# Kernel tuning notes

Hardware: AMD Instinct MI355X
Metric: run time of the kernel (lower is better)

## Reference

```python
import jax, jax.numpy as jnp
import numpy as np

B, H_IMG, W_IMG = 8, 64, 64
C, HEADS, SR, MSG = 128, 4, 4, 4
N0 = H_IMG * W_IMG


def _linear(x, w, b):
    return x @ w.T + b


def _layernorm(x, g, b, eps=1e-5):
    mu = jnp.mean(x, -1, keepdims=True)
    var = jnp.mean(jnp.square(x - mu), -1, keepdims=True)
    return (x - mu) * jax.lax.rsqrt(var + eps) * g + b


def _conv2d(x, w, b, stride, pad, groups=1):
    y = jax.lax.conv_general_dilated(
        x, w, (stride, stride), [(pad, pad), (pad, pad)],
        dimension_numbers=("NCHW", "OIHW", "NCHW"), feature_group_count=groups)
    return y + b[None, :, None, None]


def setup_inputs():
    key = jax.random.key(0)
    ks = jax.random.split(key, 16)
    def nrm(k, shape, std=0.02):
        return jax.random.normal(k, shape, jnp.float32) * std
    z = lambda *s: jnp.zeros(s, jnp.float32)
    return {
        "x": jax.random.normal(ks[0], (B, N0, C), jnp.float32),
        "msg_tokens": jax.random.normal(ks[1], (B, MSG, C), jnp.float32),
        "Wq": nrm(ks[2], (C, C)), "bq": z(C),
        "sr1_w": nrm(ks[3], (C, C, 4, 4), float(np.sqrt(2.0 / (16 * C)))), "sr1_b": z(C),
        "ln1_g": jnp.ones((C,), jnp.float32), "ln1_b": z(C),
        "sr2_w": nrm(ks[4], (C, C, 2, 2), float(np.sqrt(2.0 / (4 * C)))), "sr2_b": z(C),
        "ln2_g": jnp.ones((C,), jnp.float32), "ln2_b": z(C),
        "kv1_w": nrm(ks[5], (C, C)), "kv1_b": z(C),
        "kv2_w": nrm(ks[6], (C, C)), "kv2_b": z(C),
        "lc1_w": nrm(ks[7], (C // 2, 1, 3, 3), float(np.sqrt(2.0 / 9.0))), "lc1_b": z(C // 2),
        "lc2_w": nrm(ks[8], (C // 2, 1, 3, 3), float(np.sqrt(2.0 / 9.0))), "lc2_b": z(C // 2),
        "proj_w": nrm(ks[9], (C, C)), "proj_b": z(C),
        "H": H_IMG, "W": W_IMG,
    }


def reference(x, msg_tokens, Wq, bq, sr1_w, sr1_b, ln1_g, ln1_b,
              sr2_w, sr2_b, ln2_g, ln2_b, kv1_w, kv1_b, kv2_w, kv2_b,
              lc1_w, lc1_b, lc2_w, lc2_b, proj_w, proj_b, H, W):
    Bsz, _, Cc = x.shape
    m = msg_tokens.shape[1]
    h = HEADS
    dh = Cc // h
    scale = dh ** -0.5
    x_q = jnp.concatenate([x, msg_tokens], axis=1)       # [B, N, C]
    N = x_q.shape[1]
    q = _linear(x_q, Wq, bq).reshape(Bsz, N, h, dh).transpose(0, 2, 1, 3)  # [B,h,N,dh]
    x_img = x.transpose(0, 2, 1).reshape(Bsz, Cc, H, W)

    def branch(sr_w, sr_b, ln_g, ln_b, kv_w, kv_b, lc_w, lc_b, q_half, stride):
        Hr, Wr = H // stride, W // stride
        L = Hr * Wr
        # spatial reduction conv -> tokens
        xr = _conv2d(x_img, sr_w, sr_b, stride, 0).reshape(Bsz, Cc, L).transpose(0, 2, 1)
        # message tokens pass through the SR conv via summed weights
        msg_r = jnp.einsum('bnc,oc->bno', msg_tokens, sr_w.sum((-1, -2))) + sr_b
        xk = jax.nn.gelu(_layernorm(jnp.concatenate([xr, msg_r], 1), ln_g, ln_b), approximate=False)
        kv = _linear(xk, kv_w, kv_b).reshape(Bsz, L + m, 2, h // 2, dh).transpose(2, 0, 3, 1, 4)
        k, v = kv[0], kv[1]                               # [B, h/2, L+m, dh]
        attn = jax.nn.softmax(jnp.einsum('bhnd,bhld->bhnl', q_half, k) * scale, axis=-1)
        # fused depthwise conv on the spatial part of V (message tokens bypass)
        v_flat = v.transpose(0, 2, 1, 3).reshape(Bsz, L + m, Cc // 2).transpose(0, 2, 1)  # [B,C/2,L+m]
        lc = _conv2d(v_flat[:, :, :L].reshape(Bsz, Cc // 2, Hr, Wr), lc_w, lc_b, 1, 1,
                     groups=Cc // 2).reshape(Bsz, Cc // 2, L)
        v_add = jnp.concatenate([lc, v_flat[:, :, L:]], axis=2)
        v = v + v_add.reshape(Bsz, h // 2, dh, L + m).transpose(0, 1, 3, 2)
        return jnp.einsum('bhnl,bhld->bhnd', attn, v).transpose(0, 2, 1, 3).reshape(Bsz, N, Cc // 2)

    x1 = branch(sr1_w, sr1_b, ln1_g, ln1_b, kv1_w, kv1_b, lc1_w, lc1_b, q[:, :h // 2], SR)
    x2 = branch(sr2_w, sr2_b, ln2_g, ln2_b, kv2_w, kv2_b, lc2_w, lc2_b, q[:, h // 2:], SR // 2)
    out = _linear(jnp.concatenate([x1, x2], -1), proj_w, proj_b)
    out = x_q + out                                       # identity = x_q, drop_path = Identity
    return out[:, :-m], out[:, -m:]
```

## Files before the change

### kernel.cpp

```cpp
#include <hip/hip_runtime.h>
#include <math.h>

#define BB 8
#define CC 128
#define N0 4096
#define MSGN 4
#define NTOT 4100
#define IMG 64
#define NPAD 4112
#define QTILES 257
#define LMP1 320
#define LMP2 1088

#define OFF_WFQ    0
#define OFF_WFKV1  8192
#define OFF_WFKV2  16384
#define OFF_WFPROJ 24576
#define OFF_WFSR1  32768
#define OFF_WFSR2  163840
#define OFF_QH     196608
#define OFF_XK1    2301952
#define OFF_XK2    2435072
#define OFF_KV1O   2961408
#define OFF_KV2O   3227648
#define OFF_KH1    4280320
#define OFF_VT1    4362240
#define OFF_KH2    4444160
#define OFF_VT2    4722688
#define OFF_XP0    5001216
#define OFF_XP1    7102464
#define OFF_L0     2301952
#define OFF_L1     2433280

typedef _Float16 half8v __attribute__((ext_vector_type(8)));
typedef _Float16 half4v __attribute__((ext_vector_type(4)));
typedef float f32x4 __attribute__((ext_vector_type(4)));

__device__ __forceinline__ size_t af_idx(int m, int k, int Kc) {
    return ((size_t)((m >> 4) * Kc + (k >> 5)) * 64 + ((k >> 3) & 3) * 16 + (m & 15)) * 8 + (k & 7);
}

__global__ void prep_weights(const float* __restrict__ Wq, const float* __restrict__ kv1,
                             const float* __restrict__ kv2, const float* __restrict__ proj,
                             const float* __restrict__ sr1w, const float* __restrict__ sr2w,
                             float* __restrict__ ws, _Float16* __restrict__ Qh) {
    int u = blockIdx.x * blockDim.x + threadIdx.x;
    if (u >= 49152) {
        int idx = u - 49152;
        if (idx >= BB * 4 * (NPAD - NTOT) * 32) return;
        int d = idx & 31;
        int rest = idx >> 5;
        int n = NTOT + rest % (NPAD - NTOT);
        int rest2 = rest / (NPAD - NTOT);
        int hg = rest2 & 3;
        int b = rest2 >> 2;
        Qh[((size_t)(b * 4 + hg) * NPAD + n) * 32 + d] = (_Float16)0.f;
        return;
    }
    int seg, base;
    const float* w = nullptr;
    _Float16* dst;
    if (u < 2048)        { seg = 0; base = u;          w = Wq;   dst = (_Float16*)(ws + OFF_WFQ); }
    else if (u < 4096)   { seg = 0; base = u - 2048;   w = kv1;  dst = (_Float16*)(ws + OFF_WFKV1); }
    else if (u < 6144)   { seg = 0; base = u - 4096;   w = kv2;  dst = (_Float16*)(ws + OFF_WFKV2); }
    else if (u < 8192)   { seg = 0; base = u - 6144;   w = proj; dst = (_Float16*)(ws + OFF_WFPROJ); }
    else if (u < 40960)  { seg = 1; base = u - 8192;   w = sr1w; dst = (_Float16*)(ws + OFF_WFSR1); }
    else                 { seg = 2; base = u - 40960;  w = sr2w; dst = (_Float16*)(ws + OFF_WFSR2); }
    int lane = base & 63;
    int t = (base >> 6) & 7;
    int kc = base >> 9;
    int n = t * 16 + (lane & 15);
    int k0 = kc * 32 + (lane >> 4) * 8;
    half8v val;
    #pragma unroll
    for (int j = 0; j < 8; ++j) {
        int k = k0 + j;
        float v;
        if (seg == 0) v = w[n * 128 + k];
        else if (seg == 1) v = w[(n * 128 + (k & 127)) * 16 + (k >> 7)];
        else v = w[(n * 128 + (k & 127)) * 4 + (k >> 7)];
        val[j] = (_Float16)v;
    }
    *(half8v*)(dst + (size_t)base * 8) = val;
}

template<int S, int WR, int LL, int LM, int KW>
__device__ __forceinline__ void sr_partial(
    int mtile, int kcbase, int lane, const float* __restrict__ x,
    const float* __restrict__ msg, const _Float16* __restrict__ Wf, f32x4 acc[8]) {
    int m15 = lane & 15, quadk = lane >> 4;
    int m = mtile * 16 + m15;
    bool valid = m < BB * LM;
    const float* base = x;
    bool isimg = false;
    if (valid) {
        int b = m / LM, tok = m - b * LM;
        if (tok < LL) {
            int hr = tok / WR, wr = tok - hr * WR;
            base = x + ((size_t)b * N0 + hr * S * IMG + wr * S) * 128;
            isimg = true;
        } else {
            base = msg + ((size_t)b * MSGN + (tok - LL)) * 128;
        }
    }
    const half8v* Bp = (const half8v*)Wf + lane;
    for (int kk = 0; kk < KW; ++kk) {
        int kc = kcbase + kk;
        int k0 = (kc * 4 + quadk) * 8;
        int c = k0 & 127, ij = k0 >> 7;
        half8v a;
        if (valid) {
            int off;
            if (isimg) {
                int ki = ij / S, kj = ij - ki * S;
                off = (ki * IMG + kj) * 128 + c;
            } else off = c;
            const float4* p4 = (const float4*)(base + off);
            float4 f0 = p4[0], f1 = p4[1];
            a[0] = (_Float16)f0.x; a[1] = (_Float16)f0.y; a[2] = (_Float16)f0.z; a[3] = (_Float16)f0.w;
            a[4] = (_Float16)f1.x; a[5] = (_Float16)f1.y; a[6] = (_Float16)f1.z; a[7] = (_Float16)f1.w;
        } else {
            #pragma unroll
            for (int j = 0; j < 8; ++j) a[j] = (_Float16)0.f;
        }
        #pragma unroll
        for (int t = 0; t < 8; ++t)
            acc[t] = __builtin_amdgcn_mfma_f32_16x16x32_f16(a, Bp[(size_t)(kc * 8 + t) * 64], acc[t], 0, 0, 0);
    }
}

__global__ __launch_bounds__(256) void input_gemms(
    const float* __restrict__ x, const float* __restrict__ msg,
    const _Float16* __restrict__ Wf1, const _Float16* __restrict__ Wf2,
    const float* __restrict__ b1, const float* __restrict__ g1, const float* __restrict__ be1,
    const float* __restrict__ b2, const float* __restrict__ g2, const float* __restrict__ be2,
    _Float16* __restrict__ XK1, _Float16* __restrict__ XK2,
    const _Float16* __restrict__ WfQ, const float* __restrict__ bq,
    _Float16* __restrict__ Qh) {
    __shared__ float red[4][2048];
    int tid = threadIdx.x;
    int lane = tid & 63, wave = tid >> 6;
    int bid = blockIdx.x;

    if (bid >= 646) {
        int mt = (bid - 646) * 4 + wave;
        int m15 = lane & 15, quadk = lane >> 4;
        int m = mt * 16 + m15;
        bool valid = m < BB * NTOT;
        const float* rowp = x;
        if (valid) {
            int b = m / NTOT, n = m - b * NTOT;
            rowp = (n < N0) ? (x + ((size_t)b * N0 + n) * 128)
                            : (msg + ((size_t)b * MSGN + (n - N0)) * 128);
        }
        const half8v* Bp = (const half8v*)WfQ + lane;
        f32x4 acc[8];
        #pragma unroll
        for (int t = 0; t < 8; ++t) acc[t] = (f32x4){0.f, 0.f, 0.f, 0.f};
        #pragma unroll
        for (int kc = 0; kc < 4; ++kc) {
            half8v a;
            if (valid) {
                const float4* p4 = (const float4*)(rowp + (kc * 4 + quadk) * 8);
                float4 f0 = p4[0], f1 = p4[1];
                a[0] = (_Float16)f0.x; a[1] = (_Float16)f0.y; a[2] = (_Float16)f0.z; a[3] = (_Float16)f0.w;
                a[4] = (_Float16)f1.x; a[5] = (_Float16)f1.y; a[6] = (_Float16)f1.z; a[7] = (_Float16)f1.w;
            } else {
                #pragma unroll
                for (int j = 0; j < 8; ++j) a[j] = (_Float16)0.f;
            }
            #pragma unroll
            for (int t = 0; t < 8; ++t)
                acc[t] = __builtin_amdgcn_mfma_f32_16x16x32_f16(a, Bp[(size_t)(kc * 8 + t) * 64], acc[t], 0, 0, 0);
        }
        int quad = lane >> 4, n15 = lane & 15;
        const float qscale = 0.17677669529663687f;
        #pragma unroll
        for (int r = 0; r < 4; ++r) {
            int mm = mt * 16 + quad * 4 + r;
            if (mm >= BB * NTOT) continue;
            int b = mm / NTOT, tok = mm - b * NTOT;
            #pragma unroll
            for (int t = 0; t < 8; ++t) {
                int n = t * 16 + n15;
                Qh[((size_t)(b * 4 + (n >> 5)) * NPAD + tok) * 32 + (n & 31)] =
                    (_Float16)((acc[t][r] + bq[n]) * qscale);
            }
        }
        return;
    }

    f32x4 acc[8];
    #pragma unroll
    for (int t = 0; t < 8; ++t) acc[t] = (f32x4){0.f, 0.f, 0.f, 0.f};
    const float* bias;
    const float* lng;
    const float* lnb;
    _Float16* outp;
    int mtile, Mv;
    if (bid < 132) {
        mtile = bid; Mv = 2080;
        sr_partial<4, 16, 256, 260, 16>(mtile, wave * 16, lane, x, msg, Wf1, acc);
        bias = b1; lng = g1; lnb = be1; outp = XK1;
    } else {
        mtile = bid - 132; Mv = 8224;
        sr_partial<2, 32, 1024, 1028, 4>(mtile, wave * 4, lane, x, msg, Wf2, acc);
        bias = b2; lng = g2; lnb = be2; outp = XK2;
    }
    int quad = lane >> 4, n15 = lane & 15;
    #pragma unroll
    for (int t = 0; t < 8; ++t)
        #pragma unroll
        for (int r = 0; r < 4; ++r)
            red[wave][(quad * 4 + r) * 128 + t * 16 + n15] = acc[t][r];
    __syncthreads();
    for (int e = tid; e < 2048; e += 256)
        red[0][e] = red[0][e] + red[1][e] + red[2][e] + red[3][e];
    __syncthreads();
    int r16 = tid >> 4, l16 = tid & 15;
    int m = mtile * 16 + r16;
    float v[8];
    float s = 0.f;
    #pragma unroll
    for (int j = 0; j < 8; ++j) { v[j] = red[0][r16 * 128 + j * 16 + l16] + bias[j * 16 + l16]; s += v[j]; }
    #pragma unroll
    for (int off = 1; off < 16; off <<= 1) s += __shfl_xor(s, off);
    float mu = s * (1.f / 128.f);
    float q = 0.f;
    #pragma unroll
    for (int j = 0; j < 8; ++j) { v[j] -= mu; q += v[j] * v[j]; }
    #pragma unroll
    for (int off = 1; off < 16; off <<= 1) q += __shfl_xor(q, off);
    float rs = rsqrtf(q * (1.f / 128.f) + 1e-5f);
    if (m < Mv) {
        #pragma unroll
        for (int j = 0; j < 8; ++j) {
            int n = j * 16 + l16;
            float y = v[j] * rs * lng[n] + lnb[n];
            y = 0.5f * y * (1.f + erff(y * 0.70710678118654752f));
            outp[af_idx(m, n, 4)] = (_Float16)y;
        }
    }
}

__global__ __launch_bounds__(256) void kv_gemm(
    const _Float16* __restrict__ XK1, const _Float16* __restrict__ XK2,
    const _Float16* __restrict__ Wf1, const _Float16* __restrict__ Wf2,
    const float* __restrict__ b1, const float* __restrict__ b2,
    float* __restrict__ o1, float* __restrict__ o2) {
    int lane = threadIdx.x & 63, wave = threadIdx.x >> 6;
    int t = blockIdx.x * 4 + wave;
    int lt;
    const half8v* Ap;
    const half8v* Bp;
    const float* bias;
    float* outp;
    if (t < 130) { lt = t;       Ap = (const half8v*)XK1 + (size_t)lt * 4 * 64 + lane; Bp = (const half8v*)Wf1 + lane; bias = b1; outp = o1; }
    else         { lt = t - 130; Ap = (const half8v*)XK2 + (size_t)lt * 4 * 64 + lane; Bp = (const half8v*)Wf2 + lane; bias = b2; outp = o2; }
    f32x4 acc[8];
    #pragma unroll
    for (int tt = 0; tt < 8; ++tt) acc[tt] = (f32x4){0.f, 0.f, 0.f, 0.f};
    #pragma unroll
    for (int kc = 0; kc < 4; ++kc) {
        half8v a = Ap[(size_t)kc * 64];
        #pragma unroll
        for (int tt = 0; tt < 8; ++tt)
            acc[tt] = __builtin_amdgcn_mfma_f32_16x16x32_f16(a, Bp[(size_t)(kc * 8 + tt) * 64], acc[tt], 0, 0, 0);
    }
    int quad = lane >> 4, n15 = lane & 15;
    #pragma unroll
    for (int r = 0; r < 4; ++r) {
        int m = lt * 16 + quad * 4 + r;
        #pragma unroll
        for (int tt = 0; tt < 8; ++tt)
            outp[(size_t)m * 128 + tt * 16 + n15] = acc[tt][r] + bias[tt * 16 + n15];
    }
}

__global__ void pack_kv(const float* __restrict__ kv1o, const float* __restrict__ kv2o,
                        const float* __restrict__ lc1w, const float* __restrict__ lc1b,
                        const float* __restrict__ lc2w, const float* __restrict__ lc2b,
                        _Float16* __restrict__ Kh1, _Float16* __restrict__ Vt1,
                        _Float16* __restrict__ Kh2, _Float16* __restrict__ Vt2) {
    int idx = blockIdx.x * 256 + threadIdx.x;
    const int T1 = BB * LMP1 * 64;
    const float* kv;
    const float* lcw;
    const float* lcb;
    _Float16* Kh;
    _Float16* Vt;
    int Wr, L, Lm, Lmp, li;
    if (idx < T1) { li = idx;      kv = kv1o; lcw = lc1w; lcb = lc1b; Kh = Kh1; Vt = Vt1; Wr = 16; L = 256;  Lm = 260;  Lmp = LMP1; }
    else          { li = idx - T1; kv = kv2o; lcw = lc2w; lcb = lc2b; Kh = Kh2; Vt = Vt2; Wr = 32; L = 1024; Lm = 1028; Lmp = LMP2; }
    int ch = li & 63;
    int rest = li >> 6;
    int n = rest % Lmp;
    int b = rest / Lmp;
    int h2 = ch >> 5, d = ch & 31;
    int Hr = L / Wr;
    float kval = 0.f, vnew = 0.f;
    if (n < Lm) {
        const float* kvb = kv + (size_t)b * Lm * 128;
        kval = kvb[(size_t)n * 128 + ch];
        float v = kvb[(size_t)n * 128 + 64 + ch];
        float add;
        if (n < L) {
            int hr = n / Wr, wr = n - hr * Wr;
            float sum = lcb[ch];
            #pragma unroll
            for (int ki = 0; ki < 3; ++ki)
                #pragma unroll
                for (int kj = 0; kj < 3; ++kj) {
                    int y = hr + ki - 1, xx = wr + kj - 1;
                    if ((unsigned)y < (unsigned)Hr && (unsigned)xx < (unsigned)Wr)
                        sum += lcw[ch * 9 + ki * 3 + kj] * kvb[((size_t)y * Wr + xx) * 128 + 64 + ch];
                }
            add = sum;
        } else {
            add = v;
        }
        vnew = v + add;
    }
    Kh[((size_t)(b * 2 + h2) * Lmp + n) * 32 + d] = (_Float16)kval;
    Vt[(size_t)(b * 2 + h2) * Lmp * 32 + (size_t)(n >> 2) * 128 + d * 4 + (n & 3)] = (_Float16)vnew;
}

__global__ __launch_bounds__(256) void attn_mfma(
    const _Float16* __restrict__ Qh,
    const _Float16* __restrict__ Kh1, const _Float16* __restrict__ Vt1,
    const _Float16* __restrict__ Kh2, const _Float16* __restrict__ Vt2,
    _Float16* __restrict__ XP0, _Float16* __restrict__ XP1,
    float* __restrict__ L0, float* __restrict__ L1) {
    int tid = threadIdx.x;
    int lane = tid & 63, wave = tid >> 6;
    int b = blockIdx.y;
    int z = blockIdx.z;
    int h2 = z & 1, h = z >> 1;
    int tile = blockIdx.x * 4 + wave;
    if (tile >= QTILES) return;
    int n0 = tile * 16;
    int q16 = lane & 15, quad = lane >> 4;
    const f32x4 zf = {0.f, 0.f, 0.f, 0.f};
    _Float16* xp = h ? XP1 : XP0;
    float* Lp = h ? L1 : L0;

    for (int br = 0; br < 2; ++br) {
        int Lmp = br ? LMP2 : LMP1;
        int k_lo = h ? (br ? 576 : 192) : 0;
        int k_hi = br ? (h ? 1088 : 576) : (h ? 320 : 192);
        const _Float16* kb = (br ? Kh2 : Kh1) + (size_t)(b * 2 + h2) * Lmp * 32;
        const _Float16* vb = (br ? Vt2 : Vt1) + (size_t)(b * 2 + h2) * Lmp * 32;
        int hg = br * 2 + h2;
        half8v qf = *(const half8v*)(Qh + ((size_t)(b * 4 + hg) * NPAD + n0 + q16) * 32 + quad * 8);
        f32x4 O0 = {0.f, 0.f, 0.f, 0.f}, O1 = {0.f, 0.f, 0.f, 0.f};
        float l_part = 0.f;

        for (int k0 = k_lo; k0 < k_hi; k0 += 64) {
            f32x4 s4[4];
            #pragma unroll
            for (int i = 0; i < 4; ++i) {
                half8v kf = *(const half8v*)(kb + (size_t)(k0 + i * 16 + q16) * 32 + quad * 8);
                s4[i] = __builtin_amdgcn_mfma_f32_16x16x32_f16(kf, qf, zf, 0, 0, 0);
            }
            half4v pf[4];
            float ps = 0.f;
            #pragma unroll
            for (int i = 0; i < 4; ++i)
                #pragma unroll
                for (int r = 0; r < 4; ++r) {
                    float p = __expf(s4[i][r]);
                    ps += p;
                    pf[i][r] = (_Float16)p;
                }
            l_part += ps;
            #pragma unroll
            for (int i = 0; i < 4; ++i) {
                const _Float16* vbase = vb + (size_t)(((k0 + i * 16) >> 2) + quad) * 128 + q16 * 4;
                half4v v0 = *(const half4v*)(vbase);
                half4v v1 = *(const half4v*)(vbase + 64);
                O0 = __builtin_amdgcn_mfma_f32_16x16x16f16(pf[i], v0, O0, 0, 0, 0);
                O1 = __builtin_amdgcn_mfma_f32_16x16x16f16(pf[i], v1, O1, 0, 0, 0);
            }
        }

        float l = l_part;
        l += __shfl_xor(l, 16);
        l += __shfl_xor(l, 32);
        if (h) l -= 60.0f;
        if (quad == 0) {
            int n = n0 + q16;
            if (n < NTOT) Lp[(size_t)(b * NTOT + n) * 4 + hg] = l;
        }
        int kbase = br * 64 + h2 * 32;
        #pragma unroll
        for (int r = 0; r < 4; ++r) {
            int n = n0 + quad * 4 + r;
            if (n < NTOT) {
                int m = b * NTOT + n;
                xp[af_idx(m, kbase + q16, 4)] = (_Float16)O0[r];
                xp[af_idx(m, kbase + 16 + q16, 4)] = (_Float16)O1[r];
            }
        }
    }
}

__global__ __launch_bounds__(256) void proj_gemm(
    const _Float16* __restrict__ XP0, const _Float16* __restrict__ XP1,
    const float* __restrict__ L0, const float* __restrict__ L1,
    const _Float16* __restrict__ Wf, const float* __restrict__ bias,
    float* __restrict__ out_f32, const float* __restrict__ x, const float* __restrict__ msg) {
    int lane = threadIdx.x & 63, wave = threadIdx.x >> 6;
    int mt = blockIdx.x * 4 + wave;
    const half8v* Ap0 = (const half8v*)XP0 + (size_t)mt * 4 * 64 + lane;
    const half8v* Ap1 = (const half8v*)XP1 + (size_t)mt * 4 * 64 + lane;
    const half8v* Bp = (const half8v*)Wf + lane;
    int m15 = lane & 15;
    int mrow = mt * 16 + m15;
    bool lvalid = mrow < BB * NTOT;
    f32x4 acc[8];
    #pragma unroll
    for (int t = 0; t < 8; ++t) acc[t] = (f32x4){0.f, 0.f, 0.f, 0.f};
    #pragma unroll
    for (int kc = 0; kc < 4; ++kc) {
        half8v a0 = Ap0[(size_t)kc * 64];
        half8v a1 = Ap1[(size_t)kc * 64];
        float inv = 0.f;
        if (lvalid) {
            float l0 = L0[(size_t)mrow * 4 + kc];
            float l1 = L1[(size_t)mrow * 4 + kc];
            inv = 1.f / (l0 + l1);
        }
        half8v a;
        #pragma unroll
        for (int j = 0; j < 8; ++j)
            a[j] = (_Float16)(((float)a0[j] + (float)a1[j]) * inv);
        #pragma unroll
        for (int t = 0; t < 8; ++t)
            acc[t] = __builtin_amdgcn_mfma_f32_16x16x32_f16(a, Bp[(size_t)(kc * 8 + t) * 64], acc[t], 0, 0, 0);
    }
    int quad = lane >> 4, n15 = lane & 15;
    #pragma unroll
    for (int r = 0; r < 4; ++r) {
        int m = mt * 16 + quad * 4 + r;
        if (m >= BB * NTOT) continue;
        int b = m / NTOT, tok = m - b * NTOT;
        const float* rp;
        float* dst;
        if (tok < N0) {
            rp = x + ((size_t)b * N0 + tok) * 128;
            dst = out_f32 + ((size_t)b * N0 + tok) * 128;
        } else {
            rp = msg + ((size_t)b * MSGN + (tok - N0)) * 128;
            dst = out_f32 + (size_t)BB * N0 * 128 + ((size_t)b * MSGN + (tok - N0)) * 128;
        }
        #pragma unroll
        for (int t = 0; t < 8; ++t) {
            int n = t * 16 + n15;
            dst[n] = acc[t][r] + bias[n] + rp[n];
        }
    }
}

extern "C" void kernel_launch(void* const* d_in, const int* in_sizes, int n_in,
                              void* d_out, int out_size, void* d_ws, size_t ws_size,
                              hipStream_t stream) {
    const float* x     = (const float*)d_in[0];
    const float* msg   = (const float*)d_in[1];
    const float* Wq    = (const float*)d_in[2];
    const float* bq    = (const float*)d_in[3];
    const float* sr1w  = (const float*)d_in[4];
    const float* sr1b  = (const float*)d_in[5];
    const float* ln1g  = (const float*)d_in[6];
    const float* ln1b  = (const float*)d_in[7];
    const float* sr2w  = (const float*)d_in[8];
    const float* sr2b  = (const float*)d_in[9];
    const float* ln2g  = (const float*)d_in[10];
    const float* ln2b  = (const float*)d_in[11];
    const float* kv1w  = (const float*)d_in[12];
    const float* kv1b  = (const float*)d_in[13];
    const float* kv2w  = (const float*)d_in[14];
    const float* kv2b  = (const float*)d_in[15];
    const float* lc1w  = (const float*)d_in[16];
    const float* lc1b  = (const float*)d_in[17];
    const float* lc2w  = (const float*)d_in[18];
    const float* lc2b  = (const float*)d_in[19];
    const float* projw = (const float*)d_in[20];
    const float* projb = (const float*)d_in[21];
    float* ws  = (float*)d_ws;
    float* out = (float*)d_out;

    _Float16* WfQ    = (_Float16*)(ws + OFF_WFQ);
    _Float16* WfKV1  = (_Float16*)(ws + OFF_WFKV1);
    _Float16* WfKV2  = (_Float16*)(ws + OFF_WFKV2);
    _Float16* WfPROJ = (_Float16*)(ws + OFF_WFPROJ);
    _Float16* WfSR1  = (_Float16*)(ws + OFF_WFSR1);
    _Float16* WfSR2  = (_Float16*)(ws + OFF_WFSR2);
    _Float16* Qh     = (_Float16*)(ws + OFF_QH);
    _Float16* XP0    = (_Float16*)(ws + OFF_XP0);
    _Float16* XP1    = (_Float16*)(ws + OFF_XP1);
    float* L0        = ws + OFF_L0;
    float* L1        = ws + OFF_L1;
    _Float16* XK1    = (_Float16*)(ws + OFF_XK1);
    _Float16* XK2    = (_Float16*)(ws + OFF_XK2);
    float* kv1o      = ws + OFF_KV1O;
    float* kv2o      = ws + OFF_KV2O;
    _Float16* Kh1    = (_Float16*)(ws + OFF_KH1);
    _Float16* Vt1    = (_Float16*)(ws + OFF_VT1);
    _Float16* Kh2    = (_Float16*)(ws + OFF_KH2);
    _Float16* Vt2    = (_Float16*)(ws + OFF_VT2);

    prep_weights<<<240, 256, 0, stream>>>(Wq, kv1w, kv2w, projw, sr1w, sr2w, ws, Qh);
    input_gemms<<<1159, 256, 0, stream>>>(x, msg, WfSR1, WfSR2,
                                          sr1b, ln1g, ln1b, sr2b, ln2g, ln2b,
                                          XK1, XK2, WfQ, bq, Qh);
    kv_gemm<<<161, 256, 0, stream>>>(XK1, XK2, WfKV1, WfKV2, kv1b, kv2b, kv1o, kv2o);
    pack_kv<<<2816, 256, 0, stream>>>(kv1o, kv2o, lc1w, lc1b, lc2w, lc2b,
                                      Kh1, Vt1, Kh2, Vt2);
    attn_mfma<<<dim3(65, 8, 4), 256, 0, stream>>>(Qh, Kh1, Vt1, Kh2, Vt2,
                                                  XP0, XP1, L0, L1);
    proj_gemm<<<513, 256, 0, stream>>>(XP0, XP1, L0, L1, WfPROJ, projb, out, x, msg);
}
```

Baseline: 214.6 us.

## Process 32 queries per wave in attention, prefetch K and vectorize V loads

Each attention wave now handles two 16-row query tiles, so every K fragment and V load is reused across both tiles and the grid is halved. K fragments for the next 64-key block are loaded one iteration ahead, V is repacked in pack_kv so each lane fetches one 8-half vector instead of two 4-half loads, and softmax uses exp2 with log2(e) folded into the Q scale. Padding and workspace offsets grow to fit the larger tiles. This roughly doubles accumulator and register use per wave, which may reduce occupancy despite the launch-bounds hint.

```diff
diff --git a/kernel.cpp b/kernel.cpp
--- a/kernel.cpp
+++ b/kernel.cpp
@@ -7,8 +7,8 @@
 #define MSGN 4
 #define NTOT 4100
 #define IMG 64
-#define NPAD 4112
-#define QTILES 257
+#define NPAD 4128
+#define QT32 129
 #define LMP1 320
 #define LMP2 1088
 
@@ -19,18 +19,18 @@
 #define OFF_WFSR1  32768
 #define OFF_WFSR2  163840
 #define OFF_QH     196608
-#define OFF_XK1    2301952
-#define OFF_XK2    2435072
-#define OFF_KV1O   2961408
-#define OFF_KV2O   3227648
-#define OFF_KH1    4280320
-#define OFF_VT1    4362240
-#define OFF_KH2    4444160
-#define OFF_VT2    4722688
-#define OFF_XP0    5001216
-#define OFF_XP1    7102464
-#define OFF_L0     2301952
-#define OFF_L1     2433280
+#define OFF_XK1    2310144
+#define OFF_XK2    2443264
+#define OFF_KV1O   2969600
+#define OFF_KV2O   3235840
+#define OFF_KH1    4288512
+#define OFF_VT1    4370432
+#define OFF_KH2    4452352
+#define OFF_VT2    4730880
+#define OFF_XP0    5009408
+#define OFF_XP1    7110656
+#define OFF_L0     2310144
+#define OFF_L1     2441472
 
 typedef _Float16 half8v __attribute__((ext_vector_type(8)));
 typedef _Float16 half4v __attribute__((ext_vector_type(4)));
@@ -38,6 +38,14 @@
 
 __device__ __forceinline__ size_t af_idx(int m, int k, int Kc) {
     return ((size_t)((m >> 4) * Kc + (k >> 5)) * 64 + ((k >> 3) & 3) * 16 + (m & 15)) * 8 + (k & 7);
+}
+
+__device__ __forceinline__ float exp2_fast(float x) {
+#if __has_builtin(__builtin_amdgcn_exp2f)
+    return __builtin_amdgcn_exp2f(x);
+#else
+    return __expf(x * 0.6931471805599453f);
+#endif
 }
 
 __global__ void prep_weights(const float* __restrict__ Wq, const float* __restrict__ kv1,
@@ -174,7 +182,7 @@
                 acc[t] = __builtin_amdgcn_mfma_f32_16x16x32_f16(a, Bp[(size_t)(kc * 8 + t) * 64], acc[t], 0, 0, 0);
         }
         int quad = lane >> 4, n15 = lane & 15;
-        const float qscale = 0.17677669529663687f;
+        const float qscale = 0.17677669529663687f * 1.4426950408889634f;
         #pragma unroll
         for (int r = 0; r < 4; ++r) {
             int mm = mt * 16 + quad * 4 + r;
@@ -322,10 +330,11 @@
         vnew = v + add;
     }
     Kh[((size_t)(b * 2 + h2) * Lmp + n) * 32 + d] = (_Float16)kval;
-    Vt[(size_t)(b * 2 + h2) * Lmp * 32 + (size_t)(n >> 2) * 128 + d * 4 + (n & 3)] = (_Float16)vnew;
-}
-
-__global__ __launch_bounds__(256) void attn_mfma(
+    Vt[(size_t)(b * 2 + h2) * Lmp * 32 + (size_t)(n >> 2) * 128
+       + (d & 15) * 8 + ((d >> 4) << 2) + (n & 3)] = (_Float16)vnew;
+}
+
+__global__ __launch_bounds__(256, 4) void attn_mfma(
     const _Float16* __restrict__ Qh,
     const _Float16* __restrict__ Kh1, const _Float16* __restrict__ Vt1,
     const _Float16* __restrict__ Kh2, const _Float16* __restrict__ Vt2,
@@ -337,8 +346,8 @@
     int z = blockIdx.z;
     int h2 = z & 1, h = z >> 1;
     int tile = blockIdx.x * 4 + wave;
-    if (tile >= QTILES) return;
-    int n0 = tile * 16;
+    if (tile >= QT32) return;
+    int n0 = tile * 32;
     int q16 = lane & 15, quad = lane >> 4;
     const f32x4 zf = {0.f, 0.f, 0.f, 0.f};
     _Float16* xp = h ? XP1 : XP0;
@@ -351,45 +360,62 @@
         const _Float16* kb = (br ? Kh2 : Kh1) + (size_t)(b * 2 + h2) * Lmp * 32;
         const _Float16* vb = (br ? Vt2 : Vt1) + (size_t)(b * 2 + h2) * Lmp * 32;
         int hg = br * 2 + h2;
-        half8v qf = *(const half8v*)(Qh + ((size_t)(b * 4 + hg) * NPAD + n0 + q16) * 32 + quad * 8);
-        f32x4 O0 = {0.f, 0.f, 0.f, 0.f}, O1 = {0.f, 0.f, 0.f, 0.f};
-        float l_part = 0.f;
+        const _Float16* qp = Qh + ((size_t)(b * 4 + hg) * NPAD + n0 + q16) * 32 + quad * 8;
+        half8v qf0 = *(const half8v*)qp;
+        half8v qf1 = *(const half8v*)(qp + 512);
+        f32x4 O00 = zf, O01 = zf, O10 = zf, O11 = zf;
+        float la = 0.f, lb = 0.f;
+
+        half8v kf[4];
+        #pragma unroll
+        for (int i = 0; i < 4; ++i)
+            kf[i] = *(const half8v*)(kb + (size_t)(k_lo + i * 16 + q16) * 32 + quad * 8);
 
         for (int k0 = k_lo; k0 < k_hi; k0 += 64) {
-            f32x4 s4[4];
+            half8v vv[4];
+            #pragma unroll
+            for (int i = 0; i < 4; ++i)
+                vv[i] = *(const half8v*)(vb + (size_t)((k0 >> 2) + i * 4 + quad) * 128 + q16 * 8);
+            int k0n = (k0 + 64 < k_hi) ? k0 + 64 : k_lo;
+            half8v kn[4];
+            #pragma unroll
+            for (int i = 0; i < 4; ++i)
+                kn[i] = *(const half8v*)(kb + (size_t)(k0n + i * 16 + q16) * 32 + quad * 8);
+
+            half4v p0[4], p1[4];
             #pragma unroll
             for (int i = 0; i < 4; ++i) {
-                half8v kf = *(const half8v*)(kb + (size_t)(k0 + i * 16 + q16) * 32 + quad * 8);
-                s4[i] = __builtin_amdgcn_mfma_f32_16x16x32_f16(kf, qf, zf, 0, 0, 0);
-            }
-            half4v pf[4];
-            float ps = 0.f;
-            #pragma unroll
-            for (int i = 0; i < 4; ++i)
+                f32x4 s0 = __builtin_amdgcn_mfma_f32_16x16x32_f16(kf[i], qf0, zf, 0, 0, 0);
+                f32x4 s1 = __builtin_amdgcn_mfma_f32_16x16x32_f16(kf[i], qf1, zf, 0, 0, 0);
+                half4v a, c;
                 #pragma unroll
                 for (int r = 0; r < 4; ++r) {
-                    float p = __expf(s4[i][r]);
-                    ps += p;
-                    pf[i][r] = (_Float16)p;
+                    float e0 = exp2_fast(s0[r]); la += e0; a[r] = (_Float16)e0;
+                    float e1 = exp2_fast(s1[r]); lb += e1; c[r] = (_Float16)e1;
                 }
-            l_part += ps;
+                p0[i] = a; p1[i] = c;
+            }
             #pragma unroll
             for (int i = 0; i < 4; ++i) {
-                const _Float16* vbase = vb + (size_t)(((k0 + i * 16) >> 2) + quad) * 128 + q16 * 4;
-                half4v v0 = *(const half4v*)(vbase);
-                half4v v1 = *(const half4v*)(vbase + 64);
-                O0 = __builtin_amdgcn_mfma_f32_16x16x16f16(pf[i], v0, O0, 0, 0, 0);
-                O1 = __builtin_amdgcn_mfma_f32_16x16x16f16(pf[i], v1, O1, 0, 0, 0);
+                half4v v0 = __builtin_shufflevector(vv[i], vv[i], 0, 1, 2, 3);
+                half4v v1 = __builtin_shufflevector(vv[i], vv[i], 4, 5, 6, 7);
+                O00 = __builtin_amdgcn_mfma_f32_16x16x16f16(p0[i], v0, O00, 0, 0, 0);
+                O01 = __builtin_amdgcn_mfma_f32_16x16x16f16(p0[i], v1, O01, 0, 0, 0);
+                O10 = __builtin_amdgcn_mfma_f32_16x16x16f16(p1[i], v0, O10, 0, 0, 0);
+                O11 = __builtin_amdgcn_mfma_f32_16x16x16f16(p1[i], v1, O11, 0, 0, 0);
             }
-        }
-
-        float l = l_part;
-        l += __shfl_xor(l, 16);
-        l += __shfl_xor(l, 32);
-        if (h) l -= 60.0f;
+            #pragma unroll
+            for (int i = 0; i < 4; ++i) kf[i] = kn[i];
+        }
+
+        la += __shfl_xor(la, 16); la += __shfl_xor(la, 32);
+        lb += __shfl_xor(lb, 16); lb += __shfl_xor(lb, 32);
+        if (h) { la -= 60.0f; lb -= 60.0f; }
         if (quad == 0) {
-            int n = n0 + q16;
-            if (n < NTOT) Lp[(size_t)(b * NTOT + n) * 4 + hg] = l;
+            int na = n0 + q16;
+            if (na < NTOT) Lp[(size_t)(b * NTOT + na) * 4 + hg] = la;
+            int nb = n0 + 16 + q16;
+            if (nb < NTOT) Lp[(size_t)(b * NTOT + nb) * 4 + hg] = lb;
         }
         int kbase = br * 64 + h2 * 32;
         #pragma unroll
@@ -397,8 +423,14 @@
             int n = n0 + quad * 4 + r;
             if (n < NTOT) {
                 int m = b * NTOT + n;
-                xp[af_idx(m, kbase + q16, 4)] = (_Float16)O0[r];
-                xp[af_idx(m, kbase + 16 + q16, 4)] = (_Float16)O1[r];
+                xp[af_idx(m, kbase + q16, 4)] = (_Float16)O00[r];
+                xp[af_idx(m, kbase + 16 + q16, 4)] = (_Float16)O01[r];
+            }
+            int n2 = n + 16;
+            if (n2 < NTOT) {
+                int m = b * NTOT + n2;
+                xp[af_idx(m, kbase + q16, 4)] = (_Float16)O10[r];
+                xp[af_idx(m, kbase + 16 + q16, 4)] = (_Float16)O11[r];
             }
         }
     }
@@ -509,14 +541,14 @@
     _Float16* Kh2    = (_Float16*)(ws + OFF_KH2);
     _Float16* Vt2    = (_Float16*)(ws + OFF_VT2);
 
-    prep_weights<<<240, 256, 0, stream>>>(Wq, kv1w, kv2w, projw, sr1w, sr2w, ws, Qh);
+    prep_weights<<<304, 256, 0, stream>>>(Wq, kv1w, kv2w, projw, sr1w, sr2w, ws, Qh);
     input_gemms<<<1159, 256, 0, stream>>>(x, msg, WfSR1, WfSR2,
                                           sr1b, ln1g, ln1b, sr2b, ln2g, ln2b,
                                           XK1, XK2, WfQ, bq, Qh);
     kv_gemm<<<161, 256, 0, stream>>>(XK1, XK2, WfKV1, WfKV2, kv1b, kv2b, kv1o, kv2o);
     pack_kv<<<2816, 256, 0, stream>>>(kv1o, kv2o, lc1w, lc1b, lc2w, lc2b,
                                       Kh1, Vt1, Kh2, Vt2);
-    attn_mfma<<<dim3(65, 8, 4), 256, 0, stream>>>(Qh, Kh1, Vt1, Kh2, Vt2,
+    attn_mfma<<<dim3(33, 8, 4), 256, 0, stream>>>(Qh, Kh1, Vt1, Kh2, Vt2,
                                                   XP0, XP1, L0, L1);
     proj_gemm<<<513, 256, 0, stream>>>(XP0, XP1, L0, L1, WfPROJ, projb, out, x, msg);
 }
```

New measurement: 209.8 us. 2.2% less time.
